# Kernel optimization log

Measured on AMD Instinct MI355X. Metric: run time of the kernel, lower is better.

The kernel has to match this reference:

```python
import jax, jax.numpy as jnp
import numpy as np

DIM = 384
NUM_HEADS = 12
HEAD_DIM = DIM // NUM_HEADS
WINDOW = 7
SHIFT = 3
HIDDEN = 4 * DIM
EPS = 1e-5


def setup_inputs() -> dict:
    key = jax.random.key(0)
    ks = jax.random.split(key, 12)
    s = 0.02
    return {
        "x": jax.random.normal(ks[0], (16, DIM, 56, 56), dtype=jnp.float32),
        "norm1_w": jnp.ones((DIM,), jnp.float32),
        "norm1_b": jnp.zeros((DIM,), jnp.float32),
        "qkv_w": jax.random.normal(ks[1], (DIM, 3 * DIM), jnp.float32) * s,
        "qkv_b": jnp.zeros((3 * DIM,), jnp.float32),
        "proj_w": jax.random.normal(ks[2], (DIM, DIM), jnp.float32) * s,
        "proj_b": jnp.zeros((DIM,), jnp.float32),
        "norm2_w": jnp.ones((DIM,), jnp.float32),
        "norm2_b": jnp.zeros((DIM,), jnp.float32),
        "fc1_w": jax.random.normal(ks[3], (DIM, HIDDEN), jnp.float32) * s,
        "fc1_b": jnp.zeros((HIDDEN,), jnp.float32),
        "fc2_w": jax.random.normal(ks[4], (HIDDEN, DIM), jnp.float32) * s,
        "fc2_b": jnp.zeros((DIM,), jnp.float32),
    }


def _layer_norm(x, w, b):
    mu = jnp.mean(x, axis=-1, keepdims=True)
    var = jnp.mean(jnp.square(x - mu), axis=-1, keepdims=True)
    return (x - mu) * jax.lax.rsqrt(var + EPS) * w + b


def reference(x, norm1_w, norm1_b, qkv_w, qkv_b, proj_w, proj_b,
              norm2_w, norm2_b, fc1_w, fc1_b, fc2_w, fc2_b):
    B, C, H, W = x.shape
    ws = WINDOW
    # channel-last
    xl = jnp.transpose(x, (0, 2, 3, 1))  # [B,H,W,C]
    residual = xl
    h = _layer_norm(xl, norm1_w, norm1_b)
    if SHIFT > 0:
        h = jnp.roll(h, shift=(-SHIFT, -SHIFT), axis=(1, 2))
    # static padding (zero when H,W divisible by ws)
    pad_h = (ws - H % ws) % ws
    pad_w = (ws - W % ws) % ws
    if pad_h or pad_w:
        h = jnp.pad(h, ((0, 0), (0, pad_h), (0, pad_w), (0, 0)))
    Hp, Wp = H + pad_h, W + pad_w
    # window partition -> [nW, ws*ws, C]
    h = h.reshape(B, Hp // ws, ws, Wp // ws, ws, C)
    win = jnp.transpose(h, (0, 1, 3, 2, 4, 5)).reshape(-1, ws * ws, C)
    nW, N, _ = win.shape
    # window attention
    qkv = (win @ qkv_w + qkv_b).reshape(nW, N, 3, NUM_HEADS, HEAD_DIM)
    qkv = jnp.transpose(qkv, (2, 0, 3, 1, 4))  # [3, nW, heads, N, hd]
    q, k, v = qkv[0], qkv[1], qkv[2]
    scale = HEAD_DIM ** -0.5
    scores = jnp.einsum('whnd,whmd->whnm', q, k) * scale
    attn = jax.nn.softmax(scores, axis=-1)
    out = jnp.einsum('whnm,whmd->whnd', attn, v)
    out = jnp.transpose(out, (0, 2, 1, 3)).reshape(nW, N, C)
    out = out @ proj_w + proj_b
    # window reverse
    out = out.reshape(B, Hp // ws, Wp // ws, ws, ws, C)
    out = jnp.transpose(out, (0, 1, 3, 2, 4, 5)).reshape(B, Hp, Wp, C)
    out = out[:, :H, :W, :]
    if SHIFT > 0:
        out = jnp.roll(out, shift=(SHIFT, SHIFT), axis=(1, 2))
    xl = residual + out
    # MLP with pre-norm, exact GELU (torch default)
    m = _layer_norm(xl, norm2_w, norm2_b)
    m = jax.nn.gelu(m @ fc1_w + fc1_b, approximate=False) @ fc2_w + fc2_b
    xl = xl + m
    return jnp.transpose(xl, (0, 3, 1, 2))
```

## Files before the change

kernel.cpp:

```cpp
#include <hip/hip_runtime.h>
#include <cstdint>
#include <cstddef>

#define DIMC   384
#define NHEAD  12
#define HDIM   32
#define WSZ    7
#define NTOK   49
#define HW     56
#define SPIMG  3136
#define M_TOT  50176
#define MHALF  25088
#define HIDDEN 1536
#define WHSZ   5184

typedef __attribute__((ext_vector_type(8))) short short8;
typedef __attribute__((ext_vector_type(4))) float f32x4;

__device__ __forceinline__ short f2bf(float f) {
  uint32_t u = __builtin_bit_cast(uint32_t, f);
  u = (u + 0x7fffu + ((u >> 16) & 1u)) >> 16;
  return (short)u;
}
__device__ __forceinline__ float bf2f(short s) {
  uint32_t u = ((uint32_t)(uint16_t)s) << 16;
  return __builtin_bit_cast(float, u);
}

__device__ __forceinline__ void async16(const short* g, short* l) {
  __builtin_amdgcn_global_load_lds(
      (const __attribute__((address_space(1))) uint32_t*)g,
      (__attribute__((address_space(3))) uint32_t*)l, 16, 0, 0);
}

__global__ void wt_all_kernel(const float* __restrict__ qkv_w, const float* __restrict__ proj_w,
                              const float* __restrict__ fc1_w, const float* __restrict__ fc2_w,
                              short* __restrict__ qkvT, short* __restrict__ projT,
                              short* __restrict__ fc1T, short* __restrict__ fc2T) {
  int idx = blockIdx.x * 256 + threadIdx.x;
  const float* src; short* dst; int K, N;
  if (idx < 442368)       { src = qkv_w;  dst = qkvT;  K = 384;  N = 1152; }
  else if (idx < 589824)  { idx -= 442368; src = proj_w; dst = projT; K = 384;  N = 384; }
  else if (idx < 1179648) { idx -= 589824; src = fc1_w;  dst = fc1T;  K = 384;  N = 1536; }
  else if (idx < 1769472) { idx -= 1179648; src = fc2_w; dst = fc2T;  K = 1536; N = 384; }
  else return;
  int k = idx / N, n = idx - k * N;
  dst[(size_t)n * K + k] = f2bf(src[idx]);
}

__global__ __launch_bounds__(256) void ln1_win_kernel(const float* __restrict__ x,
                                                      const float* __restrict__ w,
                                                      const float* __restrict__ b,
                                                      float* __restrict__ xl,
                                                      short* __restrict__ win) {
  __shared__ float tile[32][385];
  int bid = blockIdx.x;
  int img = bid / 98;
  int s0  = (bid - img * 98) * 32;
  const float* xp = x + (size_t)img * DIMC * SPIMG;
  int tid = threadIdx.x;
  #pragma unroll 4
  for (int it = 0; it < 48; ++it) {
    int idx = it * 256 + tid;
    int s = idx & 31, c = idx >> 5;
    tile[s][c] = xp[(size_t)c * SPIMG + s0 + s];
  }
  __syncthreads();
  int wave = tid >> 6, lane = tid & 63;
  for (int i = 0; i < 8; ++i) {
    int sl = wave * 8 + i;
    int s  = s0 + sl;
    float v[6]; float sum = 0.f, ss = 0.f;
    #pragma unroll
    for (int j = 0; j < 6; ++j) { v[j] = tile[sl][j * 64 + lane]; sum += v[j]; ss += v[j] * v[j]; }
    #pragma unroll
    for (int o = 32; o; o >>= 1) { sum += __shfl_xor(sum, o); ss += __shfl_xor(ss, o); }
    float mu   = sum * (1.f / 384.f);
    float var  = ss * (1.f / 384.f) - mu * mu;
    float rstd = rsqrtf(var + 1e-5f);
    int h = s / HW, wc = s - h * HW;
    int ir = h - 3;  if (ir < 0) ir += HW;
    int jr = wc - 3; if (jr < 0) jr += HW;
    int widx = img * 64 + (ir / WSZ) * 8 + (jr / WSZ);
    int tok  = (ir % WSZ) * WSZ + (jr % WSZ);
    size_t spat = (size_t)img * SPIMG + s;
    float* xlr = xl + spat * DIMC;
    short* wr  = win + (size_t)(widx * NTOK + tok) * DIMC;
    #pragma unroll
    for (int j = 0; j < 6; ++j) {
      int c = j * 64 + lane;
      xlr[c] = v[j];
      wr[c]  = f2bf((v[j] - mu) * rstd * w[c] + b[c]);
    }
  }
}

__device__ __forceinline__ void gemm_core(const short* __restrict__ A, int lda,
                                          const short* __restrict__ Bt, int ldb, int K,
                                          int m0, int n0, short* sA, short* sB,
                                          f32x4 acc[4][4]) {
  const int tid = threadIdx.x;
  const int wave = tid >> 6, lane = tid & 63;
  const int wm = (wave >> 1) << 6, wn = (wave & 1) << 6;
  const int lr = lane & 15, lk = lane >> 4;
  #pragma unroll
  for (int i = 0; i < 4; ++i)
    #pragma unroll
    for (int j = 0; j < 4; ++j)
      #pragma unroll
      for (int q = 0; q < 4; ++q) acc[i][j][q] = 0.f;

  for (int kt = 0; kt < K; kt += 64) {
    #pragma unroll
    for (int r = 0; r < 4; ++r) {
      int flat = r * 256 + tid;
      int row  = flat >> 3;
      int pcol = flat & 7;
      int lcol = pcol ^ (row & 7);
      async16(A  + (size_t)(m0 + row) * lda + kt + lcol * 8, sA + flat * 8);
      async16(Bt + (size_t)(n0 + row) * ldb + kt + lcol * 8, sB + flat * 8);
    }
    __syncthreads();
    #pragma unroll
    for (int kk = 0; kk < 2; ++kk) {
      short8 a[4], bfr[4];
      #pragma unroll
      for (int i = 0; i < 4; ++i) {
        int ra = wm + i * 16 + lr;
        int sa_ = (kk * 4 + lk) ^ (ra & 7);
        a[i] = *(const short8*)(sA + ra * 64 + sa_ * 8);
        int rb = wn + i * 16 + lr;
        int sb_ = (kk * 4 + lk) ^ (rb & 7);
        bfr[i] = *(const short8*)(sB + rb * 64 + sb_ * 8);
      }
      #pragma unroll
      for (int i = 0; i < 4; ++i)
        #pragma unroll
        for (int j = 0; j < 4; ++j)
          acc[i][j] = __builtin_amdgcn_mfma_f32_16x16x32_bf16(a[i], bfr[j], acc[i][j], 0, 0, 0);
    }
    __syncthreads();
  }
}

#define EPI_PROLOGUE \
  const int tid = threadIdx.x; const int wave = tid >> 6, lane = tid & 63; \
  const int wm = (wave >> 1) << 6, wn = (wave & 1) << 6; \
  const int lr = lane & 15, lk = lane >> 4;

__global__ __launch_bounds__(256) void gemm_qkv(const short* __restrict__ A, const short* __restrict__ Bt,
                                                const float* __restrict__ bias, short* __restrict__ qkvbuf) {
  __shared__ __align__(16) short sA[8192], sB[8192];
  int nt = blockIdx.x / 392, mt = blockIdx.x - nt * 392;
  int m0 = mt << 7, n0 = nt << 7;
  f32x4 acc[4][4];
  gemm_core(A, 384, Bt, 384, 384, m0, n0, sA, sB, acc);
  EPI_PROLOGUE
  #pragma unroll
  for (int i = 0; i < 4; ++i)
    #pragma unroll
    for (int j = 0; j < 4; ++j)
      #pragma unroll
      for (int rg = 0; rg < 4; ++rg) {
        int row = m0 + wm + i * 16 + lk * 4 + rg;
        int col = n0 + wn + j * 16 + lr;
        float v = acc[i][j][rg] + bias[col];
        int which = col / 384, rem = col - which * 384;
        int hd = rem >> 5, d = rem & 31;
        int widx = row / 49, tok = row - widx * 49;
        size_t base = ((size_t)widx * 12 + hd) * WHSZ;
        if (which == 0)      qkvbuf[base + tok * 32 + d] = f2bf(v);
        else if (which == 1) qkvbuf[base + 1568 + tok * 32 + d] = f2bf(v);
        else                 qkvbuf[base + 3136 + d * 64 + tok] = f2bf(v);
      }
}

#define QSTR 40
#define VSTR 72
__global__ __launch_bounds__(256) void attn_kernel(const short* __restrict__ qkv,
                                                   short* __restrict__ attn_out) {
  __shared__ __align__(16) short sQ[64 * QSTR];
  __shared__ __align__(16) short sK[64 * QSTR];
  __shared__ __align__(16) short sVt[32 * VSTR];
  __shared__ __align__(16) short sE[64 * VSTR];
  int bx = blockIdx.x;
  int widx = bx / 12, hd = bx - widx * 12;
  int tid = threadIdx.x;
  const int w = tid >> 6, lane = tid & 63;
  const int lr = lane & 15, lk = lane >> 4;
  const short* gq = qkv + (size_t)bx * WHSZ;
  for (int i = tid; i < 196; i += 256) {
    int tok = i >> 2, d0 = (i & 3) << 3;
    *(short8*)(sQ + tok * QSTR + d0) = *(const short8*)(gq + i * 8);
    *(short8*)(sK + tok * QSTR + d0) = *(const short8*)(gq + 1568 + i * 8);
  }
  {
    int d = tid >> 3, c0 = (tid & 7) << 3;
    *(short8*)(sVt + d * VSTR + c0) = *(const short8*)(gq + 3136 + d * 64 + c0);
  }
  __syncthreads();
  for (int i = tid; i < 480; i += 256) {
    int d = i / 15, c = 49 + i - (i / 15) * 15;
    sVt[d * VSTR + c] = 0;
  }
  short8 aq = *(const short8*)(sQ + (16 * w + lr) * QSTR + lk * 8);
  f32x4 zero = {0.f, 0.f, 0.f, 0.f};
  f32x4 s4[4];
  #pragma unroll
  for (int j = 0; j < 4; ++j) {
    short8 bk = *(const short8*)(sK + (16 * j + lr) * QSTR + lk * 8);
    s4[j] = __builtin_amdgcn_mfma_f32_16x16x32_bf16(aq, bk, zero, 0, 0, 0);
  }
  float rinv[4];
  #pragma unroll
  for (int rg = 0; rg < 4; ++rg) {
    float v[4];
    #pragma unroll
    for (int j = 0; j < 4; ++j)
      v[j] = (16 * j + lr < NTOK) ? s4[j][rg] * 0.17677669529663687f : -3.0e38f;
    float m = fmaxf(fmaxf(v[0], v[1]), fmaxf(v[2], v[3]));
    #pragma unroll
    for (int o = 1; o < 16; o <<= 1) m = fmaxf(m, __shfl_xor(m, o));
    float e0 = __expf(v[0] - m), e1 = __expf(v[1] - m);
    float e2 = __expf(v[2] - m), e3 = __expf(v[3] - m);
    float sum = (e0 + e1) + (e2 + e3);
    #pragma unroll
    for (int o = 1; o < 16; o <<= 1) sum += __shfl_xor(sum, o);
    rinv[rg] = 1.f / sum;
    int erow = 16 * w + lk * 4 + rg;
    sE[erow * VSTR + lr]      = f2bf(e0);
    sE[erow * VSTR + 16 + lr] = f2bf(e1);
    sE[erow * VSTR + 32 + lr] = f2bf(e2);
    sE[erow * VSTR + 48 + lr] = f2bf(e3);
  }
  __syncthreads();
  f32x4 o4[2] = {{0.f,0.f,0.f,0.f},{0.f,0.f,0.f,0.f}};
  #pragma unroll
  for (int ks = 0; ks < 2; ++ks) {
    short8 ae = *(const short8*)(sE + (16 * w + lr) * VSTR + ks * 32 + lk * 8);
    #pragma unroll
    for (int dt = 0; dt < 2; ++dt) {
      short8 bv = *(const short8*)(sVt + (16 * dt + lr) * VSTR + ks * 32 + lk * 8);
      o4[dt] = __builtin_amdgcn_mfma_f32_16x16x32_bf16(ae, bv, o4[dt], 0, 0, 0);
    }
  }
  #pragma unroll
  for (int rg = 0; rg < 4; ++rg) {
    int row = 16 * w + lk * 4 + rg;
    if (row < NTOK) {
      size_t rowbase = ((size_t)widx * NTOK + row) * DIMC + hd * 32;
      attn_out[rowbase + lr]      = f2bf(o4[0][rg] * rinv[rg]);
      attn_out[rowbase + 16 + lr] = f2bf(o4[1][rg] * rinv[rg]);
    }
  }
}

__global__ __launch_bounds__(256) void gemm_proj(const short* __restrict__ A, const short* __restrict__ Bt,
                                                 const float* __restrict__ bias, float* __restrict__ xl) {
  __shared__ __align__(16) short sA[8192], sB[8192];
  int nt = blockIdx.x / 392, mt = blockIdx.x - nt * 392;
  int m0 = mt << 7, n0 = nt << 7;
  f32x4 acc[4][4];
  gemm_core(A, 384, Bt, 384, 384, m0, n0, sA, sB, acc);
  EPI_PROLOGUE
  #pragma unroll
  for (int i = 0; i < 4; ++i)
    #pragma unroll
    for (int j = 0; j < 4; ++j)
      #pragma unroll
      for (int rg = 0; rg < 4; ++rg) {
        int row = m0 + wm + i * 16 + lk * 4 + rg;
        int col = n0 + wn + j * 16 + lr;
        float v = acc[i][j][rg] + bias[col];
        int widx = row / 49, tok = row - widx * 49;
        int bimg = widx >> 6, wrem = widx & 63;
        int wi = wrem >> 3, wj = wrem & 7;
        int ti = tok / 7, tj = tok - ti * 7;
        int hh = wi * 7 + ti + 3; if (hh >= HW) hh -= HW;
        int ww = wj * 7 + tj + 3; if (ww >= HW) ww -= HW;
        size_t spat = (size_t)bimg * SPIMG + hh * HW + ww;
        float* p = xl + spat * DIMC + col;
        *p = *p + v;
      }
}

__global__ __launch_bounds__(256) void ln2_kernel(const float* __restrict__ xl, const float* __restrict__ w,
                                                  const float* __restrict__ b, short* __restrict__ h2) {
  int t = blockIdx.x * 4 + (threadIdx.x >> 6);
  int lane = threadIdx.x & 63;
  const float* row = xl + (size_t)t * DIMC;
  float v[6]; float sum = 0.f, ss = 0.f;
  #pragma unroll
  for (int j = 0; j < 3; ++j) {
    float2 p2 = *(const float2*)(row + j * 128 + lane * 2);
    v[2 * j] = p2.x; v[2 * j + 1] = p2.y;
    sum += p2.x + p2.y; ss += p2.x * p2.x + p2.y * p2.y;
  }
  #pragma unroll
  for (int o = 32; o; o >>= 1) { sum += __shfl_xor(sum, o); ss += __shfl_xor(ss, o); }
  float mu = sum * (1.f / 384.f);
  float var = ss * (1.f / 384.f) - mu * mu;
  float rstd = rsqrtf(var + 1e-5f);
  short* orow = h2 + (size_t)t * DIMC;
  #pragma unroll
  for (int j = 0; j < 3; ++j) {
    int c = j * 128 + lane * 2;
    short2 o2;
    o2.x = f2bf((v[2 * j] - mu) * rstd * w[c] + b[c]);
    o2.y = f2bf((v[2 * j + 1] - mu) * rstd * w[c + 1] + b[c + 1]);
    *(short2*)(orow + c) = o2;
  }
}

__global__ __launch_bounds__(256) void gemm_fc1(const short* __restrict__ A, const short* __restrict__ Bt,
                                                const float* __restrict__ bias, short* __restrict__ h3,
                                                int mbase) {
  __shared__ __align__(16) short sA[8192], sB[8192];
  int nt = blockIdx.x / 196, mt = blockIdx.x - nt * 196;
  int m0 = mbase + (mt << 7), n0 = nt << 7;
  f32x4 acc[4][4];
  gemm_core(A, 384, Bt, 384, 384, m0, n0, sA, sB, acc);
  EPI_PROLOGUE
  #pragma unroll
  for (int i = 0; i < 4; ++i)
    #pragma unroll
    for (int j = 0; j < 4; ++j)
      #pragma unroll
      for (int rg = 0; rg < 4; ++rg) {
        int row = m0 + wm + i * 16 + lk * 4 + rg;
        int col = n0 + wn + j * 16 + lr;
        float v = acc[i][j][rg] + bias[col];
        float g = 0.5f * v * (1.f + erff(v * 0.70710678118654752f));
        h3[(size_t)(row - mbase) * HIDDEN + col] = f2bf(g);
      }
}

__global__ __launch_bounds__(256) void gemm_fc2(const short* __restrict__ A, const short* __restrict__ Bt,
                                                const float* __restrict__ bias, const float* __restrict__ xl,
                                                float* __restrict__ out, int mbase) {
  __shared__ __align__(16) short sA[8192], sB[8192];
  int nt = blockIdx.x / 196, mt = blockIdx.x - nt * 196;
  int m0l = mt << 7, n0 = nt << 7;
  f32x4 acc[4][4];
  gemm_core(A, HIDDEN, Bt, HIDDEN, HIDDEN, m0l, n0, sA, sB, acc);
  EPI_PROLOGUE
  #pragma unroll
  for (int i = 0; i < 4; ++i)
    #pragma unroll
    for (int j = 0; j < 4; ++j) {
      int row0 = mbase + m0l + wm + i * 16 + lk * 4;
      int col  = n0 + wn + j * 16 + lr;
      int bimg = row0 / SPIMG;
      int s    = row0 - bimg * SPIMG;
      float bcol = bias[col];
      f32x4 vv;
      #pragma unroll
      for (int rg = 0; rg < 4; ++rg)
        vv[rg] = acc[i][j][rg] + bcol + xl[(size_t)(row0 + rg) * DIMC + col];
      *(f32x4*)(out + ((size_t)bimg * DIMC + col) * SPIMG + s) = vv;
    }
}

#define OFF_XL    0u
#define OFF_WIN   77070336u
#define OFF_QKV   115605504u
#define OFF_QKVT  243007488u
#define OFF_PROJT 243892224u
#define OFF_FC1T  244187136u
#define OFF_FC2T  245366784u
#define WS_NEEDED 246546432u

extern "C" void kernel_launch(void* const* d_in, const int* in_sizes, int n_in,
                              void* d_out, int out_size, void* d_ws, size_t ws_size,
                              hipStream_t stream) {
  if (ws_size < (size_t)WS_NEEDED) return;

  const float* x      = (const float*)d_in[0];
  const float* n1w    = (const float*)d_in[1];
  const float* n1b    = (const float*)d_in[2];
  const float* qkv_w  = (const float*)d_in[3];
  const float* qkv_b  = (const float*)d_in[4];
  const float* proj_w = (const float*)d_in[5];
  const float* proj_b = (const float*)d_in[6];
  const float* n2w    = (const float*)d_in[7];
  const float* n2b    = (const float*)d_in[8];
  const float* fc1_w  = (const float*)d_in[9];
  const float* fc1_b  = (const float*)d_in[10];
  const float* fc2_w  = (const float*)d_in[11];
  const float* fc2_b  = (const float*)d_in[12];
  float* out = (float*)d_out;

  char* ws = (char*)d_ws;
  float* xl    = (float*)(ws + OFF_XL);
  short* win   = (short*)(ws + OFF_WIN);
  short* qkvb  = (short*)(ws + OFF_QKV);
  short* h3    = (short*)(ws + OFF_QKV);
  short* qkvT  = (short*)(ws + OFF_QKVT);
  short* projT = (short*)(ws + OFF_PROJT);
  short* fc1T  = (short*)(ws + OFF_FC1T);
  short* fc2T  = (short*)(ws + OFF_FC2T);

  wt_all_kernel<<<(1769472 + 255) / 256, 256, 0, stream>>>(qkv_w, proj_w, fc1_w, fc2_w,
                                                           qkvT, projT, fc1T, fc2T);
  ln1_win_kernel<<<16 * 98, 256, 0, stream>>>(x, n1w, n1b, xl, win);
  gemm_qkv<<<392 * 9, 256, 0, stream>>>(win, qkvT, qkv_b, qkvb);
  attn_kernel<<<1024 * 12, 256, 0, stream>>>(qkvb, win);
  gemm_proj<<<392 * 3, 256, 0, stream>>>(win, projT, proj_b, xl);
  ln2_kernel<<<12544, 256, 0, stream>>>(xl, n2w, n2b, win);
  gemm_fc1<<<196 * 12, 256, 0, stream>>>(win, fc1T, fc1_b, h3, 0);
  gemm_fc2<<<196 * 3,  256, 0, stream>>>(h3, fc2T, fc2_b, xl, out, 0);
  gemm_fc1<<<196 * 12, 256, 0, stream>>>(win, fc1T, fc1_b, h3, MHALF);
  gemm_fc2<<<196 * 3,  256, 0, stream>>>(h3, fc2T, fc2_b, xl, out, MHALF);

  (void)in_sizes; (void)n_in; (void)out_size; (void)ws_size;
}
```

Before: 711.2 us.

## Keep residual in window order, store QKV row-major, swap GEMM tile order

After: 767.1 us. 1.08x slower.

```diff
diff --git a/kernel.cpp b/kernel.cpp
--- a/kernel.cpp
+++ b/kernel.cpp
@@ -12,7 +12,7 @@
 #define M_TOT  50176
 #define MHALF  25088
 #define HIDDEN 1536
-#define WHSZ   5184
+#define QKVN   1152
 
 typedef __attribute__((ext_vector_type(8))) short short8;
 typedef __attribute__((ext_vector_type(4))) float f32x4;
@@ -83,9 +83,9 @@
     int jr = wc - 3; if (jr < 0) jr += HW;
     int widx = img * 64 + (ir / WSZ) * 8 + (jr / WSZ);
     int tok  = (ir % WSZ) * WSZ + (jr % WSZ);
-    size_t spat = (size_t)img * SPIMG + s;
-    float* xlr = xl + spat * DIMC;
-    short* wr  = win + (size_t)(widx * NTOK + tok) * DIMC;
+    size_t wrow = (size_t)(widx * NTOK + tok);
+    float* xlr = xl + wrow * DIMC;
+    short* wr  = win + wrow * DIMC;
     #pragma unroll
     for (int j = 0; j < 6; ++j) {
       int c = j * 64 + lane;
@@ -149,9 +149,9 @@
   const int lr = lane & 15, lk = lane >> 4;
 
 __global__ __launch_bounds__(256) void gemm_qkv(const short* __restrict__ A, const short* __restrict__ Bt,
-                                                const float* __restrict__ bias, short* __restrict__ qkvbuf) {
+                                                const float* __restrict__ bias, short* __restrict__ qkvr) {
   __shared__ __align__(16) short sA[8192], sB[8192];
-  int nt = blockIdx.x / 392, mt = blockIdx.x - nt * 392;
+  int mt = blockIdx.x / 9, nt = blockIdx.x - mt * 9;
   int m0 = mt << 7, n0 = nt << 7;
   f32x4 acc[4][4];
   gemm_core(A, 384, Bt, 384, 384, m0, n0, sA, sB, acc);
@@ -164,23 +164,17 @@
       for (int rg = 0; rg < 4; ++rg) {
         int row = m0 + wm + i * 16 + lk * 4 + rg;
         int col = n0 + wn + j * 16 + lr;
-        float v = acc[i][j][rg] + bias[col];
-        int which = col / 384, rem = col - which * 384;
-        int hd = rem >> 5, d = rem & 31;
-        int widx = row / 49, tok = row - widx * 49;
-        size_t base = ((size_t)widx * 12 + hd) * WHSZ;
-        if (which == 0)      qkvbuf[base + tok * 32 + d] = f2bf(v);
-        else if (which == 1) qkvbuf[base + 1568 + tok * 32 + d] = f2bf(v);
-        else                 qkvbuf[base + 3136 + d * 64 + tok] = f2bf(v);
+        qkvr[(size_t)row * QKVN + col] = f2bf(acc[i][j][rg] + bias[col]);
       }
 }
 
 #define QSTR 40
 #define VSTR 72
-__global__ __launch_bounds__(256) void attn_kernel(const short* __restrict__ qkv,
+__global__ __launch_bounds__(256) void attn_kernel(const short* __restrict__ qkvr,
                                                    short* __restrict__ attn_out) {
   __shared__ __align__(16) short sQ[64 * QSTR];
   __shared__ __align__(16) short sK[64 * QSTR];
+  __shared__ __align__(16) short sVr[NTOK * QSTR];
   __shared__ __align__(16) short sVt[32 * VSTR];
   __shared__ __align__(16) short sE[64 * VSTR];
   int bx = blockIdx.x;
@@ -188,20 +182,18 @@
   int tid = threadIdx.x;
   const int w = tid >> 6, lane = tid & 63;
   const int lr = lane & 15, lk = lane >> 4;
-  const short* gq = qkv + (size_t)bx * WHSZ;
+  const short* base = qkvr + (size_t)widx * NTOK * QKVN + hd * HDIM;
   for (int i = tid; i < 196; i += 256) {
-    int tok = i >> 2, d0 = (i & 3) << 3;
-    *(short8*)(sQ + tok * QSTR + d0) = *(const short8*)(gq + i * 8);
-    *(short8*)(sK + tok * QSTR + d0) = *(const short8*)(gq + 1568 + i * 8);
-  }
-  {
-    int d = tid >> 3, c0 = (tid & 7) << 3;
-    *(short8*)(sVt + d * VSTR + c0) = *(const short8*)(gq + 3136 + d * 64 + c0);
+    int tok = i >> 2, p = (i & 3) << 3;
+    const short* rp = base + (size_t)tok * QKVN + p;
+    *(short8*)(sQ  + tok * QSTR + p) = *(const short8*)(rp);
+    *(short8*)(sK  + tok * QSTR + p) = *(const short8*)(rp + 384);
+    *(short8*)(sVr + tok * QSTR + p) = *(const short8*)(rp + 768);
   }
   __syncthreads();
-  for (int i = tid; i < 480; i += 256) {
-    int d = i / 15, c = 49 + i - (i / 15) * 15;
-    sVt[d * VSTR + c] = 0;
+  for (int e = tid; e < 2048; e += 256) {
+    int d = e >> 6, c = e & 63;
+    sVt[d * VSTR + c] = (c < NTOK) ? sVr[c * QSTR + d] : (short)0;
   }
   short8 aq = *(const short8*)(sQ + (16 * w + lr) * QSTR + lk * 8);
   f32x4 zero = {0.f, 0.f, 0.f, 0.f};
@@ -248,7 +240,7 @@
   for (int rg = 0; rg < 4; ++rg) {
     int row = 16 * w + lk * 4 + rg;
     if (row < NTOK) {
-      size_t rowbase = ((size_t)widx * NTOK + row) * DIMC + hd * 32;
+      size_t rowbase = ((size_t)widx * NTOK + row) * DIMC + hd * HDIM;
       attn_out[rowbase + lr]      = f2bf(o4[0][rg] * rinv[rg]);
       attn_out[rowbase + 16 + lr] = f2bf(o4[1][rg] * rinv[rg]);
     }
@@ -258,7 +250,7 @@
 __global__ __launch_bounds__(256) void gemm_proj(const short* __restrict__ A, const short* __restrict__ Bt,
                                                  const float* __restrict__ bias, float* __restrict__ xl) {
   __shared__ __align__(16) short sA[8192], sB[8192];
-  int nt = blockIdx.x / 392, mt = blockIdx.x - nt * 392;
+  int mt = blockIdx.x / 3, nt = blockIdx.x - mt * 3;
   int m0 = mt << 7, n0 = nt << 7;
   f32x4 acc[4][4];
   gemm_core(A, 384, Bt, 384, 384, m0, n0, sA, sB, acc);
@@ -271,16 +263,8 @@
       for (int rg = 0; rg < 4; ++rg) {
         int row = m0 + wm + i * 16 + lk * 4 + rg;
         int col = n0 + wn + j * 16 + lr;
-        float v = acc[i][j][rg] + bias[col];
-        int widx = row / 49, tok = row - widx * 49;
-        int bimg = widx >> 6, wrem = widx & 63;
-        int wi = wrem >> 3, wj = wrem & 7;
-        int ti = tok / 7, tj = tok - ti * 7;
-        int hh = wi * 7 + ti + 3; if (hh >= HW) hh -= HW;
-        int ww = wj * 7 + tj + 3; if (ww >= HW) ww -= HW;
-        size_t spat = (size_t)bimg * SPIMG + hh * HW + ww;
-        float* p = xl + spat * DIMC + col;
-        *p = *p + v;
+        float* p = xl + (size_t)row * DIMC + col;
+        *p = *p + acc[i][j][rg] + bias[col];
       }
 }
 
@@ -316,7 +300,7 @@
                                                 const float* __restrict__ bias, short* __restrict__ h3,
                                                 int mbase) {
   __shared__ __align__(16) short sA[8192], sB[8192];
-  int nt = blockIdx.x / 196, mt = blockIdx.x - nt * 196;
+  int mt = blockIdx.x / 12, nt = blockIdx.x - mt * 12;
   int m0 = mbase + (mt << 7), n0 = nt << 7;
   f32x4 acc[4][4];
   gemm_core(A, 384, Bt, 384, 384, m0, n0, sA, sB, acc);
@@ -339,7 +323,7 @@
                                                 const float* __restrict__ bias, const float* __restrict__ xl,
                                                 float* __restrict__ out, int mbase) {
   __shared__ __align__(16) short sA[8192], sB[8192];
-  int nt = blockIdx.x / 196, mt = blockIdx.x - nt * 196;
+  int mt = blockIdx.x / 3, nt = blockIdx.x - mt * 3;
   int m0l = mt << 7, n0 = nt << 7;
   f32x4 acc[4][4];
   gemm_core(A, HIDDEN, Bt, HIDDEN, HIDDEN, m0l, n0, sA, sB, acc);
@@ -347,18 +331,20 @@
   #pragma unroll
   for (int i = 0; i < 4; ++i)
     #pragma unroll
-    for (int j = 0; j < 4; ++j) {
-      int row0 = mbase + m0l + wm + i * 16 + lk * 4;
-      int col  = n0 + wn + j * 16 + lr;
-      int bimg = row0 / SPIMG;
-      int s    = row0 - bimg * SPIMG;
-      float bcol = bias[col];
-      f32x4 vv;
-      #pragma unroll
-      for (int rg = 0; rg < 4; ++rg)
-        vv[rg] = acc[i][j][rg] + bcol + xl[(size_t)(row0 + rg) * DIMC + col];
-      *(f32x4*)(out + ((size_t)bimg * DIMC + col) * SPIMG + s) = vv;
-    }
+    for (int j = 0; j < 4; ++j)
+      #pragma unroll
+      for (int rg = 0; rg < 4; ++rg) {
+        int row = mbase + m0l + wm + i * 16 + lk * 4 + rg;
+        int col = n0 + wn + j * 16 + lr;
+        float v = acc[i][j][rg] + bias[col] + xl[(size_t)row * DIMC + col];
+        int widx = row / 49, tok = row - widx * 49;
+        int bimg = widx >> 6, wrem = widx & 63;
+        int wi = wrem >> 3, wj = wrem & 7;
+        int ti = tok / 7, tj = tok - ti * 7;
+        int hh = wi * 7 + ti + 3; if (hh >= HW) hh -= HW;
+        int ww = wj * 7 + tj + 3; if (ww >= HW) ww -= HW;
+        out[((size_t)bimg * DIMC + col) * SPIMG + hh * HW + ww] = v;
+      }
 }
 
 #define OFF_XL    0u
@@ -393,7 +379,7 @@
   char* ws = (char*)d_ws;
   float* xl    = (float*)(ws + OFF_XL);
   short* win   = (short*)(ws + OFF_WIN);
-  short* qkvb  = (short*)(ws + OFF_QKV);
+  short* qkvr  = (short*)(ws + OFF_QKV);
   short* h3    = (short*)(ws + OFF_QKV);
   short* qkvT  = (short*)(ws + OFF_QKVT);
   short* projT = (short*)(ws + OFF_PROJT);
@@ -403,8 +389,8 @@
   wt_all_kernel<<<(1769472 + 255) / 256, 256, 0, stream>>>(qkv_w, proj_w, fc1_w, fc2_w,
                                                            qkvT, projT, fc1T, fc2T);
   ln1_win_kernel<<<16 * 98, 256, 0, stream>>>(x, n1w, n1b, xl, win);
-  gemm_qkv<<<392 * 9, 256, 0, stream>>>(win, qkvT, qkv_b, qkvb);
-  attn_kernel<<<1024 * 12, 256, 0, stream>>>(qkvb, win);
+  gemm_qkv<<<392 * 9, 256, 0, stream>>>(win, qkvT, qkv_b, qkvr);
+  attn_kernel<<<1024 * 12, 256, 0, stream>>>(qkvr, win);
   gemm_proj<<<392 * 3, 256, 0, stream>>>(win, projT, proj_b, xl);
   ln2_kernel<<<12544, 256, 0, stream>>>(xl, n2w, n2b, win);
   gemm_fc1<<<196 * 12, 256, 0, stream>>>(win, fc1T, fc1_b, h3, 0);
```
